# Kernel tuning notes

Measured on AMD Instinct MI355X. Metric: run time of the kernel, lower is better.

The kernel has to match this reference:

```python
import jax, jax.numpy as jnp
import numpy as np

B, T_HIST, D, H = 32768, 50, 3, 512
FUTURE = 30


def gru_cell(x, h, W_ih, W_hh, b_ih, b_hh):
    # PyTorch GRU cell math: gates ordered (r, z, n)
    gi = x @ W_ih.T + b_ih          # [B, 3H]
    gh = h @ W_hh.T + b_hh          # [B, 3H]
    i_r, i_z, i_n = jnp.split(gi, 3, axis=-1)
    h_r, h_z, h_n = jnp.split(gh, 3, axis=-1)
    r = jax.nn.sigmoid(i_r + h_r)
    z = jax.nn.sigmoid(i_z + h_z)
    n = jnp.tanh(i_n + r * h_n)
    return (1.0 - z) * n + z * h


def setup_inputs() -> dict:
    key = jax.random.key(0)
    ks = jax.random.split(key, 20)
    s = 0.04  # ~1/sqrt(H), matches PyTorch uniform init scale
    def p(k, shape):
        return jax.random.normal(k, shape, dtype=jnp.float32) * s
    return {
        "x_input": jax.random.normal(ks[0], (B, T_HIST, D), dtype=jnp.float32),
        "future_len": FUTURE,
        # encoder GRU, layer 0 (input D) and layer 1 (input H)
        "enc_W_ih0": p(ks[1], (3 * H, D)), "enc_W_hh0": p(ks[2], (3 * H, H)),
        "enc_b_ih0": p(ks[3], (3 * H,)),  "enc_b_hh0": p(ks[4], (3 * H,)),
        "enc_W_ih1": p(ks[5], (3 * H, H)), "enc_W_hh1": p(ks[6], (3 * H, H)),
        "enc_b_ih1": p(ks[7], (3 * H,)),  "enc_b_hh1": p(ks[8], (3 * H,)),
        # decoder GRU, layer 0 (input D = output_dim) and layer 1
        "dec_W_ih0": p(ks[9], (3 * H, D)), "dec_W_hh0": p(ks[10], (3 * H, H)),
        "dec_b_ih0": p(ks[11], (3 * H,)), "dec_b_hh0": p(ks[12], (3 * H,)),
        "dec_W_ih1": p(ks[13], (3 * H, H)), "dec_W_hh1": p(ks[14], (3 * H, H)),
        "dec_b_ih1": p(ks[15], (3 * H,)), "dec_b_hh1": p(ks[16], (3 * H,)),
        # output projection
        "fc_W": p(ks[17], (D, H)), "fc_b": p(ks[18], (D,)),
    }


def reference(x_input, future_len,
              enc_W_ih0, enc_W_hh0, enc_b_ih0, enc_b_hh0,
              enc_W_ih1, enc_W_hh1, enc_b_ih1, enc_b_hh1,
              dec_W_ih0, dec_W_hh0, dec_b_ih0, dec_b_hh0,
              dec_W_ih1, dec_W_hh1, dec_b_ih1, dec_b_hh1,
              fc_W, fc_b):
    b = x_input.shape[0]
    h_init = jnp.zeros((b, H), dtype=x_input.dtype)

    # ---- encoder: 2-layer GRU over history (eval mode, no dropout) ----
    def enc_step(carry, x_t):
        h0, h1 = carry
        h0 = gru_cell(x_t, h0, enc_W_ih0, enc_W_hh0, enc_b_ih0, enc_b_hh0)
        h1 = gru_cell(h0, h1, enc_W_ih1, enc_W_hh1, enc_b_ih1, enc_b_hh1)
        return (h0, h1), None

    (h0, h1), _ = jax.lax.scan(enc_step, (h_init, h_init),
                               jnp.swapaxes(x_input, 0, 1))  # [T, B, D]

    def dec_step(carry, _):
        d0, d1, xin = carry
        d0 = gru_cell(xin, d0, dec_W_ih0, dec_W_hh0, dec_b_ih0, dec_b_hh0)
        d1 = gru_cell(d0, d1, dec_W_ih1, dec_W_hh1, dec_b_ih1, dec_b_hh1)
        pred = d1 @ fc_W.T + fc_b  # [B, D]
        return (d0, d1, pred), pred

    _, outs = jax.lax.scan(dec_step, (h0, h1, x_input[:, -1, :]),
                           None, length=future_len)  # [F, B, D]
    return jnp.swapaxes(outs, 0, 1)  # [B, F, D]
```

## Files before the change

kernel.cpp:

```cpp
#include <hip/hip_runtime.h>
#include <hip/hip_fp16.h>
#include <stdint.h>

typedef _Float16 h8 __attribute__((ext_vector_type(8)));
typedef float f4 __attribute__((ext_vector_type(4)));

#define DEV static __device__ __forceinline__

constexpr int BATCH  = 32768;
constexpr int HID    = 512;
constexpr int T_HIST = 50;
constexpr int FUT    = 30;
constexpr int BM = 128, BN = 32, BK = 64;

DEV void gl2lds16(const void* g, void* l) {
  __builtin_amdgcn_global_load_lds(
      (const __attribute__((address_space(1))) void*)g,
      (__attribute__((address_space(3))) void*)l,
      16, 0, 0);
}

DEV float sigm(float x)     { return 1.f / (1.f + __expf(-x)); }
DEV float tanhfast(float x) { return 1.f - 2.f / (__expf(2.f * x) + 1.f); }

__global__ void zero_fill(float4* __restrict__ p, int n4) {
  int i = blockIdx.x * 256 + threadIdx.x;
  if (i < n4) p[i] = float4{0.f, 0.f, 0.f, 0.f};
}

__global__ void pack_w(const float* __restrict__ Wa, const float* __restrict__ Wb,
                       _Float16* __restrict__ out, int KC) {
  int i = blockIdx.x * 256 + threadIdx.x;
  int total = 16 * KC * 3 * 32 * 64;
  if (i >= total) return;
  int k0  = i & 7;
  int k8s = (i >> 3) & 7;
  int n   = (i >> 6) & 31;
  int t   = i >> 11;
  int g   = t % 3;
  int t2  = t / 3;
  int kc  = t2 % KC;
  int nb  = t2 / KC;
  int k8  = k8s ^ (n & 7);
  int row = g * 512 + nb * 32 + n;
  int kg  = kc * 64 + k8 * 8 + k0;
  float v = (kg < 512) ? Wa[(size_t)row * 512 + kg] : Wb[(size_t)row * 512 + kg - 512];
  out[i] = (_Float16)v;
}

__global__ void pack_bias(const float* __restrict__ bih, const float* __restrict__ bhh,
                          float* __restrict__ out) {
  int j = blockIdx.x * 256 + threadIdx.x;
  if (j >= 512) return;
  out[j]        = bih[j]        + bhh[j];
  out[512 + j]  = bih[512 + j]  + bhh[512 + j];
  out[1024 + j] = bih[1024 + j];
  out[1536 + j] = bhh[1024 + j];
}

__global__ void pack_wx(const float* __restrict__ Wih, float* __restrict__ out) {
  int i = blockIdx.x * 256 + threadIdx.x;
  if (i >= 512 * 9) return;
  int j = i / 9, q = i % 9, g = q / 3, k = q % 3;
  out[i] = Wih[(size_t)(g * 512 + j) * 3 + k];
}

template <int KC, bool L0>
__launch_bounds__(256, 2)
__global__ void gru_step(const _Float16* __restrict__ Bp,
                         const _Float16* __restrict__ Alo,
                         const _Float16* __restrict__ Ahi,
                         _Float16* __restrict__ hnew16,
                         const float* __restrict__ bias,
                         const float* __restrict__ Wx,
                         const float* __restrict__ xin,
                         int xstride) {
  __shared__ alignas(16) _Float16 sA[2][BM * BK];
  __shared__ alignas(16) _Float16 sB[2][3 * BN * BK];

  const int tid  = threadIdx.x;
  const int wave = tid >> 6;
  const int lane = tid & 63;
  const int quad = lane >> 4;
  const int l15  = lane & 15;
  const int L  = blockIdx.x;
  const int c  = L & 7;
  const int q  = L >> 3;
  const int cb = q & 15;
  const int rb = (c << 5) | (q >> 4);
  const int row0 = rb * BM;
  const int col0 = cb * BN;

  f4 acc_r[2][2]  = {};
  f4 acc_z[2][2]  = {};
  f4 acc_n0[2][2] = {};
  f4 acc_n1[2][2] = {};

  const _Float16* Bblk = Bp + (size_t)cb * KC * (3 * BN * BK);

  auto stage = [&](int kcs, int buf) {
    const _Float16* Asrc = (KC == 16 && kcs >= 8) ? Ahi : Alo;
    const int kb = (kcs & 7) * BK;
#pragma unroll
    for (int i = 0; i < 4; ++i) {
      int ga = wave * 256 + i * 64 + lane;
      int m = ga >> 3, k8s = ga & 7;
      int k8l = k8s ^ (m & 7);
      gl2lds16(Asrc + (size_t)(row0 + m) * HID + kb + k8l * 8,
               &sA[buf][(wave * 256 + i * 64) * 8]);
    }
    const _Float16* Bsrc = Bblk + (size_t)kcs * (3 * BN * BK);
#pragma unroll
    for (int i = 0; i < 3; ++i) {
      int gb = wave * 192 + i * 64 + lane;
      gl2lds16(Bsrc + (size_t)gb * 8, &sB[buf][(wave * 192 + i * 64) * 8]);
    }
  };

  stage(0, 0);
  asm volatile("s_waitcnt vmcnt(0)" ::: "memory");
  __builtin_amdgcn_s_barrier();

  for (int kc = 0; kc < KC; ++kc) {
    const int buf = kc & 1;
    if (kc + 1 < KC) stage(kc + 1, buf ^ 1);

    const _Float16* sAc = sA[buf];
    const _Float16* sBc = sB[buf];
#pragma unroll
    for (int s = 0; s < 2; ++s) {
      const int sw = ((s * 4 + quad) ^ (l15 & 7)) * 8;
      h8 af[2];
#pragma unroll
      for (int mt = 0; mt < 2; ++mt)
        af[mt] = *(const h8*)&sAc[(wave * 32 + mt * 16 + l15) * BK + sw];
#pragma unroll
      for (int nt = 0; nt < 2; ++nt) {
        const int nrow = nt * 16 + l15;
        h8 br = *(const h8*)&sBc[(0 * BN + nrow) * BK + sw];
        h8 bz = *(const h8*)&sBc[(1 * BN + nrow) * BK + sw];
        h8 bn = *(const h8*)&sBc[(2 * BN + nrow) * BK + sw];
#pragma unroll
        for (int mt = 0; mt < 2; ++mt) {
          acc_r[mt][nt] = __builtin_amdgcn_mfma_f32_16x16x32_f16(af[mt], br, acc_r[mt][nt], 0, 0, 0);
          acc_z[mt][nt] = __builtin_amdgcn_mfma_f32_16x16x32_f16(af[mt], bz, acc_z[mt][nt], 0, 0, 0);
          if (L0 || kc >= 8)
            acc_n1[mt][nt] = __builtin_amdgcn_mfma_f32_16x16x32_f16(af[mt], bn, acc_n1[mt][nt], 0, 0, 0);
          else
            acc_n0[mt][nt] = __builtin_amdgcn_mfma_f32_16x16x32_f16(af[mt], bn, acc_n0[mt][nt], 0, 0, 0);
        }
      }
    }
    asm volatile("s_waitcnt vmcnt(0)" ::: "memory");
    __builtin_amdgcn_s_barrier();
  }

  const _Float16* hold16 = L0 ? Alo : Ahi;
  float bR[2], bZ[2], bI[2], bH[2];
  float wx[2][9];
#pragma unroll
  for (int nt = 0; nt < 2; ++nt) {
    int j = col0 + nt * 16 + l15;
    bR[nt] = bias[j];
    bZ[nt] = bias[512 + j];
    bI[nt] = bias[1024 + j];
    bH[nt] = bias[1536 + j];
    if constexpr (L0) {
#pragma unroll
      for (int q2 = 0; q2 < 9; ++q2) wx[nt][q2] = Wx[j * 9 + q2];
    }
  }
  float xv[2][4][3];
  if constexpr (L0) {
#pragma unroll
    for (int mt = 0; mt < 2; ++mt)
#pragma unroll
      for (int r = 0; r < 4; ++r) {
        int b = row0 + wave * 32 + mt * 16 + quad * 4 + r;
        const float* xp = xin + (size_t)b * xstride;
        xv[mt][r][0] = xp[0]; xv[mt][r][1] = xp[1]; xv[mt][r][2] = xp[2];
      }
  }
#pragma unroll
  for (int mt = 0; mt < 2; ++mt) {
#pragma unroll
    for (int r = 0; r < 4; ++r) {
      int b = row0 + wave * 32 + mt * 16 + quad * 4 + r;
#pragma unroll
      for (int nt = 0; nt < 2; ++nt) {
        int j = col0 + nt * 16 + l15;
        size_t idx = (size_t)b * HID + j;
        float rr = acc_r[mt][nt][r] + bR[nt];
        float zz = acc_z[mt][nt][r] + bZ[nt];
        float hn = acc_n1[mt][nt][r] + bH[nt];
        float in_;
        if constexpr (L0) {
          const float* w = wx[nt];
          rr += xv[mt][r][0] * w[0] + xv[mt][r][1] * w[1] + xv[mt][r][2] * w[2];
          zz += xv[mt][r][0] * w[3] + xv[mt][r][1] * w[4] + xv[mt][r][2] * w[5];
          in_ = bI[nt] + xv[mt][r][0] * w[6] + xv[mt][r][1] * w[7] + xv[mt][r][2] * w[8];
        } else {
          in_ = acc_n0[mt][nt][r] + bI[nt];
        }
        float rg = sigm(rr);
        float zg = sigm(zz);
        float ng = tanhfast(in_ + rg * hn);
        float hp = (float)hold16[idx];
        float hv = (1.f - zg) * ng + zg * hp;
        hnew16[idx] = (_Float16)hv;
      }
    }
  }
}

__global__ __launch_bounds__(256) void fc_kernel(const _Float16* __restrict__ h,
                                                 const float* __restrict__ W,
                                                 const float* __restrict__ bfc,
                                                 float* __restrict__ out) {
  int wave = threadIdx.x >> 6, lane = threadIdx.x & 63;
  int b = blockIdx.x * 4 + wave;
  const h8* hp = (const h8*)(h + (size_t)b * 512);
  h8 a0 = hp[lane];
  float s[3];
#pragma unroll
  for (int d = 0; d < 3; ++d) {
    const float4* wp = (const float4*)(W + d * 512);
    float4 w0 = wp[lane * 2], w1 = wp[lane * 2 + 1];
    s[d] = (float)a0[0] * w0.x + (float)a0[1] * w0.y + (float)a0[2] * w0.z + (float)a0[3] * w0.w
         + (float)a0[4] * w1.x + (float)a0[5] * w1.y + (float)a0[6] * w1.z + (float)a0[7] * w1.w;
  }
#pragma unroll
  for (int d = 0; d < 3; ++d)
#pragma unroll
    for (int off = 32; off > 0; off >>= 1) s[d] += __shfl_xor(s[d], off, 64);
  if (lane == 0) {
    out[(size_t)b * 90 + 0] = s[0] + bfc[0];
    out[(size_t)b * 90 + 1] = s[1] + bfc[1];
    out[(size_t)b * 90 + 2] = s[2] + bfc[2];
  }
}

extern "C" void kernel_launch(void* const* d_in, const int* in_sizes, int n_in,
                              void* d_out, int out_size, void* d_ws, size_t ws_size,
                              hipStream_t stream) {
  (void)in_sizes; (void)n_in; (void)out_size; (void)ws_size;
  const float* x_input = (const float*)d_in[0];
  const float* eWih0 = (const float*)d_in[2];
  const float* eWhh0 = (const float*)d_in[3];
  const float* ebih0 = (const float*)d_in[4];
  const float* ebhh0 = (const float*)d_in[5];
  const float* eWih1 = (const float*)d_in[6];
  const float* eWhh1 = (const float*)d_in[7];
  const float* ebih1 = (const float*)d_in[8];
  const float* ebhh1 = (const float*)d_in[9];
  const float* dWih0 = (const float*)d_in[10];
  const float* dWhh0 = (const float*)d_in[11];
  const float* dbih0 = (const float*)d_in[12];
  const float* dbhh0 = (const float*)d_in[13];
  const float* dWih1 = (const float*)d_in[14];
  const float* dWhh1 = (const float*)d_in[15];
  const float* dbih1 = (const float*)d_in[16];
  const float* dbhh1 = (const float*)d_in[17];
  const float* fcW   = (const float*)d_in[18];
  const float* fcb   = (const float*)d_in[19];
  float* out = (float*)d_out;

  char* ws = (char*)d_ws;
  const size_t S16 = (size_t)BATCH * HID * 2;
  _Float16* h0h[2] = {(_Float16*)(ws),            (_Float16*)(ws + S16)};
  _Float16* h1h[2] = {(_Float16*)(ws + 2 * S16),  (_Float16*)(ws + 3 * S16)};
  char* p = ws + 4 * S16;
  const size_t W8  = (size_t)16 * 8  * 3 * 32 * 64 * 2;
  const size_t W16 = (size_t)16 * 16 * 3 * 32 * 64 * 2;
  _Float16* pkE0 = (_Float16*)p; p += W8;
  _Float16* pkE1 = (_Float16*)p; p += W16;
  _Float16* pkD0 = (_Float16*)p; p += W8;
  _Float16* pkD1 = (_Float16*)p; p += W16;
  float* bE0 = (float*)p; p += 2048 * 4;
  float* bE1 = (float*)p; p += 2048 * 4;
  float* bD0 = (float*)p; p += 2048 * 4;
  float* bD1 = (float*)p; p += 2048 * 4;
  float* wxE = (float*)p; p += 512 * 9 * 4;
  float* wxD = (float*)p; p += 512 * 9 * 4;

  pack_w<<<dim3(3072), 256, 0, stream>>>(eWhh0, eWhh0, pkE0, 8);
  pack_w<<<dim3(6144), 256, 0, stream>>>(eWih1, eWhh1, pkE1, 16);
  pack_w<<<dim3(3072), 256, 0, stream>>>(dWhh0, dWhh0, pkD0, 8);
  pack_w<<<dim3(6144), 256, 0, stream>>>(dWih1, dWhh1, pkD1, 16);
  pack_bias<<<2, 256, 0, stream>>>(ebih0, ebhh0, bE0);
  pack_bias<<<2, 256, 0, stream>>>(ebih1, ebhh1, bE1);
  pack_bias<<<2, 256, 0, stream>>>(dbih0, dbhh0, bD0);
  pack_bias<<<2, 256, 0, stream>>>(dbih1, dbhh1, bD1);
  pack_wx<<<18, 256, 0, stream>>>(eWih0, wxE);
  pack_wx<<<18, 256, 0, stream>>>(dWih0, wxD);

  {
    int n4 = (int)(S16 / 16);
    zero_fill<<<(n4 + 255) / 256, 256, 0, stream>>>((float4*)h0h[0], n4);
    zero_fill<<<(n4 + 255) / 256, 256, 0, stream>>>((float4*)h1h[0], n4);
  }

  dim3 grid(4096), blk(256);
  int p0 = 0, p1 = 0;
  for (int t = 0; t < T_HIST; ++t) {
    gru_step<8, true><<<grid, blk, 0, stream>>>(pkE0, h0h[p0], nullptr,
                                                h0h[1 - p0], bE0, wxE,
                                                x_input + (size_t)t * 3, 150);
    p0 ^= 1;
    gru_step<16, false><<<grid, blk, 0, stream>>>(pkE1, h0h[p0], h1h[p1],
                                                  h1h[1 - p1], bE1, nullptr, nullptr, 0);
    p1 ^= 1;
  }
  for (int t = 0; t < FUT; ++t) {
    const float* xp; int xs;
    if (t == 0) { xp = x_input + (size_t)49 * 3; xs = 150; }
    else        { xp = out + (size_t)(t - 1) * 3; xs = 90; }
    gru_step<8, true><<<grid, blk, 0, stream>>>(pkD0, h0h[p0], nullptr,
                                                h0h[1 - p0], bD0, wxD, xp, xs);
    p0 ^= 1;
    gru_step<16, false><<<grid, blk, 0, stream>>>(pkD1, h0h[p0], h1h[p1],
                                                  h1h[1 - p1], bD1, nullptr, nullptr, 0);
    p1 ^= 1;
    fc_kernel<<<8192, 256, 0, stream>>>(h1h[p1], fcW, fcb, out + (size_t)t * 3);
  }
}
```

Baseline: 18.70 ms.

## Use triple-buffered BK=32 LDS pipeline with wave-specialized loads in GRU step

Halves the K tile to 32 and switches from double to triple buffering in a single shared LDS array, so stage s+2 is issued while stage s is computed. Partial vmcnt waits replace full drains. Waves 0-1 load the activation tile and waves 2-3 load the weight tile. Weight packing and the swizzle are adapted to the 32-wide K chunks, and launch bounds now request 3 blocks per CU to fit the smaller LDS footprint. The cost is twice as many barriers per GEMM and more per-wave load imbalance.

```diff
diff --git a/kernel.cpp b/kernel.cpp
--- a/kernel.cpp
+++ b/kernel.cpp
@@ -11,7 +11,8 @@
 constexpr int HID    = 512;
 constexpr int T_HIST = 50;
 constexpr int FUT    = 30;
-constexpr int BM = 128, BN = 32, BK = 64;
+constexpr int BM = 128, BN = 32, BK = 32;
+constexpr int SLOT_H = BM * BK + 3 * BN * BK;
 
 DEV void gl2lds16(const void* g, void* l) {
   __builtin_amdgcn_global_load_lds(
@@ -29,21 +30,21 @@
 }
 
 __global__ void pack_w(const float* __restrict__ Wa, const float* __restrict__ Wb,
-                       _Float16* __restrict__ out, int KC) {
+                       _Float16* __restrict__ out, int KC32) {
   int i = blockIdx.x * 256 + threadIdx.x;
-  int total = 16 * KC * 3 * 32 * 64;
+  int total = 16 * KC32 * 3 * 32 * 32;
   if (i >= total) return;
   int k0  = i & 7;
-  int k8s = (i >> 3) & 7;
-  int n   = (i >> 6) & 31;
-  int t   = i >> 11;
+  int gs  = (i >> 3) & 3;
+  int n   = (i >> 5) & 31;
+  int t   = i >> 10;
   int g   = t % 3;
   int t2  = t / 3;
-  int kc  = t2 % KC;
-  int nb  = t2 / KC;
-  int k8  = k8s ^ (n & 7);
+  int kc  = t2 % KC32;
+  int nb  = t2 / KC32;
+  int gl  = gs ^ ((n >> 1) & 3);
   int row = g * 512 + nb * 32 + n;
-  int kg  = kc * 64 + k8 * 8 + k0;
+  int kg  = kc * 32 + gl * 8 + k0;
   float v = (kg < 512) ? Wa[(size_t)row * 512 + kg] : Wb[(size_t)row * 512 + kg - 512];
   out[i] = (_Float16)v;
 }
@@ -65,8 +66,8 @@
   out[i] = Wih[(size_t)(g * 512 + j) * 3 + k];
 }
 
-template <int KC, bool L0>
-__launch_bounds__(256, 2)
+template <int KC32, bool L0>
+__launch_bounds__(256, 3)
 __global__ void gru_step(const _Float16* __restrict__ Bp,
                          const _Float16* __restrict__ Alo,
                          const _Float16* __restrict__ Ahi,
@@ -75,8 +76,7 @@
                          const float* __restrict__ Wx,
                          const float* __restrict__ xin,
                          int xstride) {
-  __shared__ alignas(16) _Float16 sA[2][BM * BK];
-  __shared__ alignas(16) _Float16 sB[2][3 * BN * BK];
+  __shared__ alignas(16) _Float16 lds[3 * SLOT_H];
 
   const int tid  = threadIdx.x;
   const int wave = tid >> 6;
@@ -96,63 +96,79 @@
   f4 acc_n0[2][2] = {};
   f4 acc_n1[2][2] = {};
 
-  const _Float16* Bblk = Bp + (size_t)cb * KC * (3 * BN * BK);
-
-  auto stage = [&](int kcs, int buf) {
-    const _Float16* Asrc = (KC == 16 && kcs >= 8) ? Ahi : Alo;
-    const int kb = (kcs & 7) * BK;
-#pragma unroll
-    for (int i = 0; i < 4; ++i) {
-      int ga = wave * 256 + i * 64 + lane;
-      int m = ga >> 3, k8s = ga & 7;
-      int k8l = k8s ^ (m & 7);
-      gl2lds16(Asrc + (size_t)(row0 + m) * HID + kb + k8l * 8,
-               &sA[buf][(wave * 256 + i * 64) * 8]);
-    }
-    const _Float16* Bsrc = Bblk + (size_t)kcs * (3 * BN * BK);
-#pragma unroll
-    for (int i = 0; i < 3; ++i) {
-      int gb = wave * 192 + i * 64 + lane;
-      gl2lds16(Bsrc + (size_t)gb * 8, &sB[buf][(wave * 192 + i * 64) * 8]);
+  const _Float16* Bblk = Bp + (size_t)cb * KC32 * 3072;
+
+  auto stage = [&](int kcs, int slot) {
+    _Float16* base = &lds[slot * SLOT_H];
+    if (wave < 2) {
+      const _Float16* Asrc = (KC32 == 32 && kcs >= 16) ? Ahi : Alo;
+      const int kb = (kcs & 15) * BK;
+#pragma unroll
+      for (int i = 0; i < 4; ++i) {
+        int si = i * 128 + wave * 64 + lane;
+        int m  = si >> 2, gsv = si & 3;
+        int gl = gsv ^ ((m >> 1) & 3);
+        gl2lds16(Asrc + (size_t)(row0 + m) * HID + kb + gl * 8,
+                 base + (i * 128 + wave * 64) * 8);
+      }
+    } else {
+      const _Float16* Bsrc = Bblk + (size_t)kcs * 3072;
+#pragma unroll
+      for (int i = 0; i < 3; ++i) {
+        int off = i * 128 + (wave - 2) * 64;
+        gl2lds16(Bsrc + (size_t)(off + lane) * 8,
+                 base + BM * BK + off * 8);
+      }
     }
   };
 
   stage(0, 0);
-  asm volatile("s_waitcnt vmcnt(0)" ::: "memory");
-  __builtin_amdgcn_s_barrier();
-
-  for (int kc = 0; kc < KC; ++kc) {
-    const int buf = kc & 1;
-    if (kc + 1 < KC) stage(kc + 1, buf ^ 1);
-
-    const _Float16* sAc = sA[buf];
-    const _Float16* sBc = sB[buf];
-#pragma unroll
-    for (int s = 0; s < 2; ++s) {
-      const int sw = ((s * 4 + quad) ^ (l15 & 7)) * 8;
-      h8 af[2];
-#pragma unroll
-      for (int mt = 0; mt < 2; ++mt)
-        af[mt] = *(const h8*)&sAc[(wave * 32 + mt * 16 + l15) * BK + sw];
-#pragma unroll
-      for (int nt = 0; nt < 2; ++nt) {
-        const int nrow = nt * 16 + l15;
-        h8 br = *(const h8*)&sBc[(0 * BN + nrow) * BK + sw];
-        h8 bz = *(const h8*)&sBc[(1 * BN + nrow) * BK + sw];
-        h8 bn = *(const h8*)&sBc[(2 * BN + nrow) * BK + sw];
-#pragma unroll
-        for (int mt = 0; mt < 2; ++mt) {
-          acc_r[mt][nt] = __builtin_amdgcn_mfma_f32_16x16x32_f16(af[mt], br, acc_r[mt][nt], 0, 0, 0);
-          acc_z[mt][nt] = __builtin_amdgcn_mfma_f32_16x16x32_f16(af[mt], bz, acc_z[mt][nt], 0, 0, 0);
-          if (L0 || kc >= 8)
-            acc_n1[mt][nt] = __builtin_amdgcn_mfma_f32_16x16x32_f16(af[mt], bn, acc_n1[mt][nt], 0, 0, 0);
-          else
-            acc_n0[mt][nt] = __builtin_amdgcn_mfma_f32_16x16x32_f16(af[mt], bn, acc_n0[mt][nt], 0, 0, 0);
-        }
-      }
-    }
-    asm volatile("s_waitcnt vmcnt(0)" ::: "memory");
+  stage(1, 1);
+
+  int sl = 0;
+  int st = 2;
+  for (int s = 0; s < KC32; ++s) {
+    if (s + 2 < KC32) stage(s + 2, st);
+    int ahead = KC32 - 1 - s; if (ahead > 2) ahead = 2;
+    if (wave < 2) {
+      if (ahead == 2)      asm volatile("s_waitcnt vmcnt(8)" ::: "memory");
+      else if (ahead == 1) asm volatile("s_waitcnt vmcnt(4)" ::: "memory");
+      else                 asm volatile("s_waitcnt vmcnt(0)" ::: "memory");
+    } else {
+      if (ahead == 2)      asm volatile("s_waitcnt vmcnt(6)" ::: "memory");
+      else if (ahead == 1) asm volatile("s_waitcnt vmcnt(3)" ::: "memory");
+      else                 asm volatile("s_waitcnt vmcnt(0)" ::: "memory");
+    }
     __builtin_amdgcn_s_barrier();
+    __builtin_amdgcn_sched_barrier(0);
+
+    const _Float16* sAc = &lds[sl * SLOT_H];
+    const _Float16* sBc = sAc + BM * BK;
+    const int sw = (quad ^ ((l15 >> 1) & 3)) * 8;
+    h8 af[2];
+#pragma unroll
+    for (int mt = 0; mt < 2; ++mt)
+      af[mt] = *(const h8*)&sAc[(wave * 32 + mt * 16 + l15) * BK + sw];
+#pragma unroll
+    for (int nt = 0; nt < 2; ++nt) {
+      const int nrow = nt * 16 + l15;
+      h8 br = *(const h8*)&sBc[(0 * BN + nrow) * BK + sw];
+      h8 bz = *(const h8*)&sBc[(1 * BN + nrow) * BK + sw];
+      h8 bn = *(const h8*)&sBc[(2 * BN + nrow) * BK + sw];
+#pragma unroll
+      for (int mt = 0; mt < 2; ++mt) {
+        acc_r[mt][nt] = __builtin_amdgcn_mfma_f32_16x16x32_f16(af[mt], br, acc_r[mt][nt], 0, 0, 0);
+        acc_z[mt][nt] = __builtin_amdgcn_mfma_f32_16x16x32_f16(af[mt], bz, acc_z[mt][nt], 0, 0, 0);
+        if (L0 || s >= 16)
+          acc_n1[mt][nt] = __builtin_amdgcn_mfma_f32_16x16x32_f16(af[mt], bn, acc_n1[mt][nt], 0, 0, 0);
+        else
+          acc_n0[mt][nt] = __builtin_amdgcn_mfma_f32_16x16x32_f16(af[mt], bn, acc_n0[mt][nt], 0, 0, 0);
+      }
+    }
+    __builtin_amdgcn_sched_barrier(0);
+    __builtin_amdgcn_s_barrier();
+    sl = (sl == 2) ? 0 : sl + 1;
+    st = (st == 2) ? 0 : st + 1;
   }
 
   const _Float16* hold16 = L0 ? Alo : Ahi;
@@ -270,8 +286,8 @@
   _Float16* h0h[2] = {(_Float16*)(ws),            (_Float16*)(ws + S16)};
   _Float16* h1h[2] = {(_Float16*)(ws + 2 * S16),  (_Float16*)(ws + 3 * S16)};
   char* p = ws + 4 * S16;
-  const size_t W8  = (size_t)16 * 8  * 3 * 32 * 64 * 2;
-  const size_t W16 = (size_t)16 * 16 * 3 * 32 * 64 * 2;
+  const size_t W8  = (size_t)16 * 16 * 3 * 32 * 32 * 2;
+  const size_t W16 = (size_t)16 * 32 * 3 * 32 * 32 * 2;
   _Float16* pkE0 = (_Float16*)p; p += W8;
   _Float16* pkE1 = (_Float16*)p; p += W16;
   _Float16* pkD0 = (_Float16*)p; p += W8;
@@ -283,10 +299,10 @@
   float* wxE = (float*)p; p += 512 * 9 * 4;
   float* wxD = (float*)p; p += 512 * 9 * 4;
 
-  pack_w<<<dim3(3072), 256, 0, stream>>>(eWhh0, eWhh0, pkE0, 8);
-  pack_w<<<dim3(6144), 256, 0, stream>>>(eWih1, eWhh1, pkE1, 16);
-  pack_w<<<dim3(3072), 256, 0, stream>>>(dWhh0, dWhh0, pkD0, 8);
-  pack_w<<<dim3(6144), 256, 0, stream>>>(dWih1, dWhh1, pkD1, 16);
+  pack_w<<<dim3(3072), 256, 0, stream>>>(eWhh0, eWhh0, pkE0, 16);
+  pack_w<<<dim3(6144), 256, 0, stream>>>(eWih1, eWhh1, pkE1, 32);
+  pack_w<<<dim3(3072), 256, 0, stream>>>(dWhh0, dWhh0, pkD0, 16);
+  pack_w<<<dim3(6144), 256, 0, stream>>>(dWih1, dWhh1, pkD1, 32);
   pack_bias<<<2, 256, 0, stream>>>(ebih0, ebhh0, bE0);
   pack_bias<<<2, 256, 0, stream>>>(ebih1, ebhh1, bE1);
   pack_bias<<<2, 256, 0, stream>>>(dbih0, dbhh0, bD0);
@@ -303,11 +319,11 @@
   dim3 grid(4096), blk(256);
   int p0 = 0, p1 = 0;
   for (int t = 0; t < T_HIST; ++t) {
-    gru_step<8, true><<<grid, blk, 0, stream>>>(pkE0, h0h[p0], nullptr,
-                                                h0h[1 - p0], bE0, wxE,
-                                                x_input + (size_t)t * 3, 150);
+    gru_step<16, true><<<grid, blk, 0, stream>>>(pkE0, h0h[p0], nullptr,
+                                                 h0h[1 - p0], bE0, wxE,
+                                                 x_input + (size_t)t * 3, 150);
     p0 ^= 1;
-    gru_step<16, false><<<grid, blk, 0, stream>>>(pkE1, h0h[p0], h1h[p1],
+    gru_step<32, false><<<grid, blk, 0, stream>>>(pkE1, h0h[p0], h1h[p1],
                                                   h1h[1 - p1], bE1, nullptr, nullptr, 0);
     p1 ^= 1;
   }
@@ -315,10 +331,10 @@
     const float* xp; int xs;
     if (t == 0) { xp = x_input + (size_t)49 * 3; xs = 150; }
     else        { xp = out + (size_t)(t - 1) * 3; xs = 90; }
-    gru_step<8, true><<<grid, blk, 0, stream>>>(pkD0, h0h[p0], nullptr,
-                                                h0h[1 - p0], bD0, wxD, xp, xs);
+    gru_step<16, true><<<grid, blk, 0, stream>>>(pkD0, h0h[p0], nullptr,
+                                                 h0h[1 - p0], bD0, wxD, xp, xs);
     p0 ^= 1;
-    gru_step<16, false><<<grid, blk, 0, stream>>>(pkD1, h0h[p0], h1h[p1],
+    gru_step<32, false><<<grid, blk, 0, stream>>>(pkD1, h0h[p0], h1h[p1],
                                                   h1h[1 - p1], bD1, nullptr, nullptr, 0);
     p1 ^= 1;
     fc_kernel<<<8192, 256, 0, stream>>>(h1h[p1], fcW, fcb, out + (size_t)t * 3);
```

New measurement: 19.05 ms. No clear change (+1.9%).

## Enlarge GRU GEMM tile to 256 rows with triple-buffered LDS pipeline

Applied to the files above, without the earlier changes.

Doubles the block row tile to 256 using 512-thread blocks, so each B (weight) tile staged in LDS is shared by twice as many rows. The double buffer becomes a 3-slot ring that prefetches two k-steps ahead, with A and B loads split across the two half-steps. Ping-pong barriers with s_setprio are added around the MFMA bursts. This targets load latency and weight traffic, but adds more barriers, uses more LDS per block, and may lower occupancy. The epilogue has to handle 8 waves correctly.

```diff
diff --git a/kernel.cpp b/kernel.cpp
--- a/kernel.cpp
+++ b/kernel.cpp
@@ -11,7 +11,8 @@
 constexpr int HID    = 512;
 constexpr int T_HIST = 50;
 constexpr int FUT    = 30;
-constexpr int BM = 128, BN = 32, BK = 64;
+constexpr int BM = 256, BN = 32, BK = 64;
+constexpr int SLOT = BM * BK + 3 * BN * BK;
 
 DEV void gl2lds16(const void* g, void* l) {
   __builtin_amdgcn_global_load_lds(
@@ -66,7 +67,7 @@
 }
 
 template <int KC, bool L0>
-__launch_bounds__(256, 2)
+__launch_bounds__(512, 2)
 __global__ void gru_step(const _Float16* __restrict__ Bp,
                          const _Float16* __restrict__ Alo,
                          const _Float16* __restrict__ Ahi,
@@ -75,8 +76,7 @@
                          const float* __restrict__ Wx,
                          const float* __restrict__ xin,
                          int xstride) {
-  __shared__ alignas(16) _Float16 sA[2][BM * BK];
-  __shared__ alignas(16) _Float16 sB[2][3 * BN * BK];
+  __shared__ alignas(16) _Float16 lds[3 * SLOT];
 
   const int tid  = threadIdx.x;
   const int wave = tid >> 6;
@@ -87,7 +87,7 @@
   const int c  = L & 7;
   const int q  = L >> 3;
   const int cb = q & 15;
-  const int rb = (c << 5) | (q >> 4);
+  const int rb = (c << 4) | (q >> 4);
   const int row0 = rb * BM;
   const int col0 = cb * BN;
 
@@ -98,61 +98,92 @@
 
   const _Float16* Bblk = Bp + (size_t)cb * KC * (3 * BN * BK);
 
-  auto stage = [&](int kcs, int buf) {
+  auto stageA = [&](int kcs, int slot) {
     const _Float16* Asrc = (KC == 16 && kcs >= 8) ? Ahi : Alo;
     const int kb = (kcs & 7) * BK;
+    _Float16* base = &lds[slot * SLOT];
 #pragma unroll
     for (int i = 0; i < 4; ++i) {
       int ga = wave * 256 + i * 64 + lane;
       int m = ga >> 3, k8s = ga & 7;
       int k8l = k8s ^ (m & 7);
       gl2lds16(Asrc + (size_t)(row0 + m) * HID + kb + k8l * 8,
-               &sA[buf][(wave * 256 + i * 64) * 8]);
-    }
+               base + (size_t)(wave * 256 + i * 64) * 8);
+    }
+  };
+  auto stageB = [&](int kcs, int slot) {
     const _Float16* Bsrc = Bblk + (size_t)kcs * (3 * BN * BK);
+    _Float16* base = &lds[slot * SLOT] + BM * BK;
 #pragma unroll
     for (int i = 0; i < 3; ++i) {
-      int gb = wave * 192 + i * 64 + lane;
-      gl2lds16(Bsrc + (size_t)gb * 8, &sB[buf][(wave * 192 + i * 64) * 8]);
+      int gb = wave * 192 + i * 64;
+      gl2lds16(Bsrc + (size_t)(gb + lane) * 8, base + (size_t)gb * 8);
     }
   };
 
-  stage(0, 0);
-  asm volatile("s_waitcnt vmcnt(0)" ::: "memory");
+  stageA(0, 0); if (wave < 4) stageB(0, 0);
+  stageA(1, 1); if (wave < 4) stageB(1, 1);
+  if (wave < 4) asm volatile("s_waitcnt vmcnt(7)" ::: "memory");
+  else          asm volatile("s_waitcnt vmcnt(4)" ::: "memory");
   __builtin_amdgcn_s_barrier();
-
-  for (int kc = 0; kc < KC; ++kc) {
-    const int buf = kc & 1;
-    if (kc + 1 < KC) stage(kc + 1, buf ^ 1);
-
-    const _Float16* sAc = sA[buf];
-    const _Float16* sBc = sB[buf];
-#pragma unroll
-    for (int s = 0; s < 2; ++s) {
-      const int sw = ((s * 4 + quad) ^ (l15 & 7)) * 8;
-      h8 af[2];
-#pragma unroll
-      for (int mt = 0; mt < 2; ++mt)
-        af[mt] = *(const h8*)&sAc[(wave * 32 + mt * 16 + l15) * BK + sw];
-#pragma unroll
-      for (int nt = 0; nt < 2; ++nt) {
-        const int nrow = nt * 16 + l15;
-        h8 br = *(const h8*)&sBc[(0 * BN + nrow) * BK + sw];
-        h8 bz = *(const h8*)&sBc[(1 * BN + nrow) * BK + sw];
-        h8 bn = *(const h8*)&sBc[(2 * BN + nrow) * BK + sw];
-#pragma unroll
-        for (int mt = 0; mt < 2; ++mt) {
-          acc_r[mt][nt] = __builtin_amdgcn_mfma_f32_16x16x32_f16(af[mt], br, acc_r[mt][nt], 0, 0, 0);
-          acc_z[mt][nt] = __builtin_amdgcn_mfma_f32_16x16x32_f16(af[mt], bz, acc_z[mt][nt], 0, 0, 0);
-          if (L0 || kc >= 8)
-            acc_n1[mt][nt] = __builtin_amdgcn_mfma_f32_16x16x32_f16(af[mt], bn, acc_n1[mt][nt], 0, 0, 0);
-          else
-            acc_n0[mt][nt] = __builtin_amdgcn_mfma_f32_16x16x32_f16(af[mt], bn, acc_n0[mt][nt], 0, 0, 0);
+  __builtin_amdgcn_sched_barrier(0);
+
+  int cur = 0, nx2 = 2;
+  for (int s = 0; s < KC; ++s) {
+    const _Float16* sAc = &lds[cur * SLOT];
+    const _Float16* sBc = sAc + BM * BK;
+#pragma unroll
+    for (int sh = 0; sh < 2; ++sh) {
+      const int sw = ((sh * 4 + quad) ^ (l15 & 7)) * 8;
+      h8 af0 = *(const h8*)&sAc[(wave * 32 + 0 * 16 + l15) * BK + sw];
+      h8 af1 = *(const h8*)&sAc[(wave * 32 + 1 * 16 + l15) * BK + sw];
+      h8 br0 = *(const h8*)&sBc[(0 * BN + 0 * 16 + l15) * BK + sw];
+      h8 bz0 = *(const h8*)&sBc[(1 * BN + 0 * 16 + l15) * BK + sw];
+      h8 bn0 = *(const h8*)&sBc[(2 * BN + 0 * 16 + l15) * BK + sw];
+      h8 br1 = *(const h8*)&sBc[(0 * BN + 1 * 16 + l15) * BK + sw];
+      h8 bz1 = *(const h8*)&sBc[(1 * BN + 1 * 16 + l15) * BK + sw];
+      h8 bn1 = *(const h8*)&sBc[(2 * BN + 1 * 16 + l15) * BK + sw];
+      if (s + 2 < KC) {
+        if (sh == 0) stageA(s + 2, nx2);
+        else if (wave < 4) stageB(s + 2, nx2);
+      }
+      __builtin_amdgcn_s_barrier();
+      __builtin_amdgcn_sched_barrier(0);
+      __builtin_amdgcn_s_setprio(1);
+      acc_r[0][0] = __builtin_amdgcn_mfma_f32_16x16x32_f16(af0, br0, acc_r[0][0], 0, 0, 0);
+      acc_r[1][0] = __builtin_amdgcn_mfma_f32_16x16x32_f16(af1, br0, acc_r[1][0], 0, 0, 0);
+      acc_r[0][1] = __builtin_amdgcn_mfma_f32_16x16x32_f16(af0, br1, acc_r[0][1], 0, 0, 0);
+      acc_r[1][1] = __builtin_amdgcn_mfma_f32_16x16x32_f16(af1, br1, acc_r[1][1], 0, 0, 0);
+      acc_z[0][0] = __builtin_amdgcn_mfma_f32_16x16x32_f16(af0, bz0, acc_z[0][0], 0, 0, 0);
+      acc_z[1][0] = __builtin_amdgcn_mfma_f32_16x16x32_f16(af1, bz0, acc_z[1][0], 0, 0, 0);
+      acc_z[0][1] = __builtin_amdgcn_mfma_f32_16x16x32_f16(af0, bz1, acc_z[0][1], 0, 0, 0);
+      acc_z[1][1] = __builtin_amdgcn_mfma_f32_16x16x32_f16(af1, bz1, acc_z[1][1], 0, 0, 0);
+      if (L0 || s >= 8) {
+        acc_n1[0][0] = __builtin_amdgcn_mfma_f32_16x16x32_f16(af0, bn0, acc_n1[0][0], 0, 0, 0);
+        acc_n1[1][0] = __builtin_amdgcn_mfma_f32_16x16x32_f16(af1, bn0, acc_n1[1][0], 0, 0, 0);
+        acc_n1[0][1] = __builtin_amdgcn_mfma_f32_16x16x32_f16(af0, bn1, acc_n1[0][1], 0, 0, 0);
+        acc_n1[1][1] = __builtin_amdgcn_mfma_f32_16x16x32_f16(af1, bn1, acc_n1[1][1], 0, 0, 0);
+      } else {
+        acc_n0[0][0] = __builtin_amdgcn_mfma_f32_16x16x32_f16(af0, bn0, acc_n0[0][0], 0, 0, 0);
+        acc_n0[1][0] = __builtin_amdgcn_mfma_f32_16x16x32_f16(af1, bn0, acc_n0[1][0], 0, 0, 0);
+        acc_n0[0][1] = __builtin_amdgcn_mfma_f32_16x16x32_f16(af0, bn1, acc_n0[0][1], 0, 0, 0);
+        acc_n0[1][1] = __builtin_amdgcn_mfma_f32_16x16x32_f16(af1, bn1, acc_n0[1][1], 0, 0, 0);
+      }
+      __builtin_amdgcn_s_setprio(0);
+      if (sh == 1 && s + 1 < KC) {
+        if (s + 2 < KC) {
+          if (wave < 4) asm volatile("s_waitcnt vmcnt(7)" ::: "memory");
+          else          asm volatile("s_waitcnt vmcnt(4)" ::: "memory");
+        } else {
+          asm volatile("s_waitcnt vmcnt(0)" ::: "memory");
         }
       }
-    }
-    asm volatile("s_waitcnt vmcnt(0)" ::: "memory");
-    __builtin_amdgcn_s_barrier();
+      __builtin_amdgcn_sched_barrier(0);
+      __builtin_amdgcn_s_barrier();
+      __builtin_amdgcn_sched_barrier(0);
+    }
+    cur = (cur == 2) ? 0 : cur + 1;
+    nx2 = (nx2 == 2) ? 0 : nx2 + 1;
   }
 
   const _Float16* hold16 = L0 ? Alo : Ahi;
@@ -300,7 +331,7 @@
     zero_fill<<<(n4 + 255) / 256, 256, 0, stream>>>((float4*)h1h[0], n4);
   }
 
-  dim3 grid(4096), blk(256);
+  dim3 grid(2048), blk(512);
   int p0 = 0, p1 = 0;
   for (int t = 0; t < T_HIST; ++t) {
     gru_step<8, true><<<grid, blk, 0, stream>>>(pkE0, h0h[p0], nullptr,
```

Measured after the change: 18.70 ms. Within noise of the previous version (+0.0%).
